# Performance work log

Measured on AMD Instinct MI355X. Metric: run time of the kernel, lower is better.

## Reference

```python
import jax, jax.numpy as jnp
import numpy as np

EPS = 0.1  # entropic regularization epsilon
N, F, R, H = 512, 32, 8, 128


def setup_inputs() -> dict:
    key = jax.random.key(0)
    ks = jax.random.split(key, 9)
    s0 = 1.0 / np.sqrt(F + R)
    sh = 1.0 / np.sqrt(H)
    return {
        "X": jax.random.normal(ks[0], (N, F), jnp.float32),
        "U": jax.random.normal(ks[1], (N, R), jnp.float32),
        "Y": jax.random.normal(ks[2], (N, R), jnp.float32),
        "Wx": jax.random.normal(ks[3], (F, H), jnp.float32) * s0,
        "Wy": jax.random.normal(ks[4], (R, H), jnp.float32) * s0,
        "b0": jnp.zeros((H,), jnp.float32),
        "W1": jax.random.normal(ks[5], (H, H), jnp.float32) * sh,
        "b1": jnp.zeros((H,), jnp.float32),
        "W2": jax.random.normal(ks[6], (H, H), jnp.float32) * sh,
        "b2": jnp.zeros((H,), jnp.float32),
        "Wout": jax.random.normal(ks[7], (H, 1), jnp.float32) * sh,
        "bout": jnp.zeros((1,), jnp.float32),
    }


def _mlp_tail(h, W1, b1, W2, b2, Wout, bout):
    h = jax.nn.softplus(h @ W1 + b1)
    h = jax.nn.softplus(h @ W2 + b2)
    return h @ Wout + bout  # [..., 1]


def reference(X, U, Y, Wx, Wy, b0, W1, b1, W2, b2, Wout, bout):
    n = X.shape[0]
    # ---- estimate_psi (potential net estimates 'y' side directly) ----
    h_row = jax.nn.softplus(X @ Wx + Y @ Wy + b0)              # [n, H]
    psi = _mlp_tail(h_row, W1, b1, W2, b2, Wout, bout)         # [n, 1]
    # ---- estimate_phi: entropic dual over all (X_i, Y_j) pairs ----
    # First-layer pre-activation built by broadcast-sum instead of concat.
    h_pair = jax.nn.softplus((X @ Wx)[:, None, :] + (Y @ Wy)[None, :, :] + b0)  # [n, n, H]
    psi_vals = _mlp_tail(h_pair, W1, b1, W2, b2, Wout, bout)[..., 0]            # [n, n]
    cost = U @ Y.T                                             # [n, n]
    slack = cost - psi_vals
    m = jnp.max(slack, axis=1, keepdims=True)                  # [n, 1]
    lme = jax.nn.logsumexp((slack - m) / EPS, axis=1, keepdims=True) \
          - jnp.log(jnp.asarray(n, slack.dtype)) + m / EPS
    phi = EPS * lme                                            # [n, 1]
    return jnp.mean(phi) + jnp.mean(psi)
```

## Files before the change

### kernel.cpp

```cpp
#include <hip/hip_runtime.h>
#include <hip/hip_bf16.h>
#include <math.h>

#define NN 512
#define HH 128
#define FF 32
#define RR 8
#define EPSV 0.1f
#define INV_EPS 10.0f
#define LOG2E 1.4426950408889634f
#define LN2 0.6931471805599453f
#define K2E (INV_EPS * LOG2E)

typedef unsigned short ushort_t;
typedef __attribute__((ext_vector_type(8))) short bf16x8;
typedef __attribute__((ext_vector_type(4))) float f32x4;
typedef __attribute__((ext_vector_type(4))) unsigned int u32x4;
typedef __attribute__((ext_vector_type(2))) unsigned int u32x2;

__device__ __forceinline__ float g2(float t) {
    return fmaxf(t, 0.f) + __log2f(1.f + __builtin_amdgcn_exp2f(-fabsf(t)));
}
__device__ __forceinline__ ushort_t f2b(float f) {
    unsigned u = __float_as_uint(f);
    return (ushort_t)((u + 0x7fffu + ((u >> 16) & 1u)) >> 16);
}
__device__ __forceinline__ float b2f(ushort_t h) {
    return __uint_as_float(((unsigned)h) << 16);
}
__device__ __forceinline__ unsigned pk2(float a, float b) {
    __hip_bfloat162 h = __float22bfloat162_rn(make_float2(a, b));
    return *reinterpret_cast<unsigned*>(&h);
}

__global__ __launch_bounds__(256) void prep_kernel(
    const float* __restrict__ X, const float* __restrict__ Y,
    const float* __restrict__ Wx, const float* __restrict__ Wy,
    const float* __restrict__ b0, const float* __restrict__ W1, const float* __restrict__ W2,
    const float* __restrict__ b1, const float* __restrict__ b2, const float* __restrict__ Wout,
    ushort_t* __restrict__ Wt1b, ushort_t* __restrict__ Wt2b,
    ushort_t* __restrict__ XWxb, ushort_t* __restrict__ YWyb,
    float* __restrict__ b1e, float* __restrict__ b2e, float* __restrict__ WoutE) {
    int gid = blockIdx.x * 256 + threadIdx.x;
    if (gid < 32768) {
        int sel = gid >> 14;
        int idx = gid & 16383;
        int n = idx >> 7, k = idx & 127;
        (sel ? Wt2b : Wt1b)[idx] = f2b((sel ? W2 : W1)[k * HH + n]);
    } else if (gid < 98304) {
        int g = gid - 32768;
        int i = g >> 7, h = g & 127;
        float s = b0[h];
#pragma unroll
        for (int f = 0; f < FF; ++f) s += X[i * FF + f] * Wx[f * HH + h];
        XWxb[g] = f2b(s * LOG2E);
    } else if (gid < 163840) {
        int g = gid - 98304;
        int i = g >> 7, h = g & 127;
        float s = 0.f;
#pragma unroll
        for (int r = 0; r < RR; ++r) s += Y[i * RR + r] * Wy[r * HH + h];
        YWyb[g] = f2b(s * LOG2E);
    } else if (gid < 163968) {
        b1e[gid - 163840] = b1[gid - 163840] * LOG2E;
    } else if (gid < 164096) {
        b2e[gid - 163968] = b2[gid - 163968] * LOG2E;
    } else if (gid < 164224) {
        WoutE[gid - 164096] = Wout[gid - 164096] * LN2;
    }
}

__device__ __forceinline__ void layer_flip(
    const ushort_t* __restrict__ Hin, const ushort_t* __restrict__ WtG,
    const float* __restrict__ bias, f32x4 acc[2][4], int r16, int g4, int wv) {
    const int hbase = wv * 32 + g4 * 4;
#pragma unroll
    for (int mt = 0; mt < 2; ++mt) {
        float4 bb = *(const float4*)&bias[hbase + mt * 16];
#pragma unroll
        for (int nt = 0; nt < 4; ++nt) {
            acc[mt][nt][0] = bb.x; acc[mt][nt][1] = bb.y;
            acc[mt][nt][2] = bb.z; acc[mt][nt][3] = bb.w;
        }
    }
    bf16x8 afr[2][4];
#pragma unroll
    for (int mt = 0; mt < 2; ++mt)
#pragma unroll
        for (int ks = 0; ks < 4; ++ks)
            afr[mt][ks] = *(const bf16x8*)&WtG[(wv * 32 + mt * 16 + r16) * HH + ks * 32 + g4 * 8];
#pragma unroll
    for (int ks = 0; ks < 4; ++ks) {
        const int kb = ks * 32 + g4 * 8;
#pragma unroll
        for (int nt = 0; nt < 4; ++nt) {
            const int j = nt * 16 + r16;
            bf16x8 bfr = *(const bf16x8*)&Hin[j * HH + (kb ^ ((j & 7) << 3))];
            acc[0][nt] = __builtin_amdgcn_mfma_f32_16x16x32_bf16(afr[0][ks], bfr, acc[0][nt], 0, 0, 0);
            acc[1][nt] = __builtin_amdgcn_mfma_f32_16x16x32_bf16(afr[1][ks], bfr, acc[1][nt], 0, 0, 0);
        }
    }
}

__global__ __launch_bounds__(256, 2) void pair_kernel(
    const ushort_t* __restrict__ XWxb, const ushort_t* __restrict__ YWyb,
    const ushort_t* __restrict__ Wt1b, const ushort_t* __restrict__ Wt2b,
    const float* __restrict__ U, const float* __restrict__ Y,
    const float* __restrict__ b1e, const float* __restrict__ b2e,
    const float* __restrict__ WoutE, const float* __restrict__ bout,
    float* __restrict__ psi_arr, float* __restrict__ Mp, float* __restrict__ Sp) {
    __shared__ ushort_t Hs0[64 * HH];
    __shared__ ushort_t Hs1[64 * HH];
    __shared__ float psum[4][64];

    const int i = blockIdx.x;
    const int half = blockIdx.y;
    const int t = threadIdx.x;
    const int wv = t >> 6;
    const int r16 = t & 15;
    const int g4 = (t >> 4) & 3;
    const int srow = t >> 4;
    const float boutv = bout[0];

    float axf[8];
    {
        bf16x8 axv = *(const bf16x8*)&XWxb[i * HH + r16 * 8];
#pragma unroll
        for (int e = 0; e < 8; ++e) axf[e] = b2f((ushort_t)axv[e]);
    }
    float costr[4];
    {
        const float4 u0 = *(const float4*)&U[i * RR];
        const float4 u1 = *(const float4*)&U[i * RR + 4];
#pragma unroll
        for (int c = 0; c < 4; ++c) {
            const int j = half * 256 + c * 64 + (t & 63);
            const float4 y0 = *(const float4*)&Y[j * RR];
            const float4 y1 = *(const float4*)&Y[j * RR + 4];
            costr[c] = u0.x * y0.x + u0.y * y0.y + u0.z * y0.z + u0.w * y0.w +
                       u1.x * y1.x + u1.y * y1.y + u1.z * y1.z + u1.w * y1.w;
        }
    }
    bf16x8 afr1[2][4];
#pragma unroll
    for (int mt = 0; mt < 2; ++mt)
#pragma unroll
        for (int ks = 0; ks < 4; ++ks)
            afr1[mt][ks] = *(const bf16x8*)&Wt1b[(wv * 32 + mt * 16 + r16) * HH + ks * 32 + g4 * 8];
    float4 bias1h[2];
    bias1h[0] = *(const float4*)&b1e[wv * 32 + g4 * 4];
    bias1h[1] = *(const float4*)&b1e[wv * 32 + 16 + g4 * 4];
    float4 woutr[2];
    woutr[0] = *(const float4*)&WoutE[wv * 32 + g4 * 4];
    woutr[1] = *(const float4*)&WoutE[wv * 32 + 16 + g4 * 4];

    float m_l = -INFINITY, s_l = 0.f;
    f32x4 acc[2][4];
    bf16x8 pf[4];

#pragma unroll
    for (int s = 0; s < 4; ++s)
        pf[s] = *(const bf16x8*)&YWyb[(half * 256 + s * 16 + srow) * HH + r16 * 8];

#pragma unroll
    for (int c = 0; c < 4; ++c) {
        const int j0 = half * 256 + c * 64;
#pragma unroll
        for (int s = 0; s < 4; ++s) {
            const int p = s * 16 + srow;
            const bf16x8 yv = pf[s];
            unsigned pk[4];
#pragma unroll
            for (int e = 0; e < 4; ++e) {
                float v0 = g2(axf[2 * e]     + b2f((ushort_t)yv[2 * e]));
                float v1 = g2(axf[2 * e + 1] + b2f((ushort_t)yv[2 * e + 1]));
                pk[e] = pk2(v0, v1);
            }
            *(u32x4*)&Hs0[p * HH + ((r16 ^ (p & 7)) << 3)] = *(u32x4*)pk;
        }
        __syncthreads();
        if (c < 3) {
#pragma unroll
            for (int s = 0; s < 4; ++s)
                pf[s] = *(const bf16x8*)&YWyb[(j0 + 64 + s * 16 + srow) * HH + r16 * 8];
        }
#pragma unroll
        for (int mt = 0; mt < 2; ++mt)
#pragma unroll
            for (int nt = 0; nt < 4; ++nt) {
                acc[mt][nt][0] = bias1h[mt].x; acc[mt][nt][1] = bias1h[mt].y;
                acc[mt][nt][2] = bias1h[mt].z; acc[mt][nt][3] = bias1h[mt].w;
            }
#pragma unroll
        for (int ks = 0; ks < 4; ++ks) {
            const int kb = ks * 32 + g4 * 8;
#pragma unroll
            for (int nt = 0; nt < 4; ++nt) {
                const int j = nt * 16 + r16;
                bf16x8 bfr = *(const bf16x8*)&Hs0[j * HH + (kb ^ ((j & 7) << 3))];
                acc[0][nt] = __builtin_amdgcn_mfma_f32_16x16x32_bf16(afr1[0][ks], bfr, acc[0][nt], 0, 0, 0);
                acc[1][nt] = __builtin_amdgcn_mfma_f32_16x16x32_bf16(afr1[1][ks], bfr, acc[1][nt], 0, 0, 0);
            }
        }
#pragma unroll
        for (int mt = 0; mt < 2; ++mt) {
            const int hb = wv * 32 + mt * 16 + g4 * 4;
#pragma unroll
            for (int nt = 0; nt < 4; ++nt) {
                const int j = nt * 16 + r16;
                u32x2 wv2;
                wv2[0] = pk2(g2(acc[mt][nt][0]), g2(acc[mt][nt][1]));
                wv2[1] = pk2(g2(acc[mt][nt][2]), g2(acc[mt][nt][3]));
                *(u32x2*)&Hs1[j * HH + (hb ^ ((j & 7) << 3))] = wv2;
            }
        }
        __syncthreads();
        layer_flip(Hs1, Wt2b, b2e, acc, r16, g4, wv);
        {
            float part[4] = {0.f, 0.f, 0.f, 0.f};
#pragma unroll
            for (int mt = 0; mt < 2; ++mt) {
                const float wr[4] = {woutr[mt].x, woutr[mt].y, woutr[mt].z, woutr[mt].w};
#pragma unroll
                for (int r = 0; r < 4; ++r) {
                    const float wgt = wr[r];
#pragma unroll
                    for (int nt = 0; nt < 4; ++nt)
                        part[nt] += g2(acc[mt][nt][r]) * wgt;
                }
            }
#pragma unroll
            for (int nt = 0; nt < 4; ++nt) {
                part[nt] += __shfl_xor(part[nt], 16);
                part[nt] += __shfl_xor(part[nt], 32);
            }
            if (g4 == 0) {
#pragma unroll
                for (int nt = 0; nt < 4; ++nt) psum[wv][nt * 16 + r16] = part[nt];
            }
        }
        __syncthreads();
        if (t < 64) {
            const float psi = boutv + psum[0][t] + psum[1][t] + psum[2][t] + psum[3][t];
            const int j = j0 + t;
            const float sv = costr[c] - psi;
            const float mn = fmaxf(m_l, sv);
            s_l = s_l * __builtin_amdgcn_exp2f((m_l - mn) * K2E) +
                  __builtin_amdgcn_exp2f((sv - mn) * K2E);
            m_l = mn;
            if (j == i) psi_arr[i] = psi;
        }
    }
    if (t < 64) {
        float M = m_l;
#pragma unroll
        for (int o = 1; o < 64; o <<= 1) M = fmaxf(M, __shfl_xor(M, o));
        float S = s_l * __builtin_amdgcn_exp2f((m_l - M) * K2E);
#pragma unroll
        for (int o = 1; o < 64; o <<= 1) S += __shfl_xor(S, o);
        if (t == 0) {
            Mp[i * 2 + half] = M;
            Sp[i * 2 + half] = S;
        }
    }
}

__global__ __launch_bounds__(512) void finalize_kernel(
    const float* __restrict__ psi_arr, const float* __restrict__ Mp,
    const float* __restrict__ Sp, float* __restrict__ out) {
    __shared__ float red[8];
    const int t = threadIdx.x;
    const float M0 = Mp[2 * t], M1 = Mp[2 * t + 1];
    const float S0 = Sp[2 * t], S1 = Sp[2 * t + 1];
    const float Mg = fmaxf(M0, M1);
    const float S = S0 * __expf((M0 - Mg) * INV_EPS) + S1 * __expf((M1 - Mg) * INV_EPS);
    const float phi = EPSV * (__logf(S) - __logf((float)NN)) + Mg;
    float v = phi + psi_arr[t];
#pragma unroll
    for (int o = 1; o < 64; o <<= 1) v += __shfl_xor(v, o);
    if ((t & 63) == 0) red[t >> 6] = v;
    __syncthreads();
    if (t == 0) {
        float tot = 0.f;
#pragma unroll
        for (int w = 0; w < 8; ++w) tot += red[w];
        out[0] = tot / (float)NN;
    }
}

extern "C" void kernel_launch(void* const* d_in, const int* in_sizes, int n_in,
                              void* d_out, int out_size, void* d_ws, size_t ws_size,
                              hipStream_t stream) {
    (void)in_sizes; (void)n_in; (void)out_size; (void)ws_size;
    const float* X    = (const float*)d_in[0];
    const float* U    = (const float*)d_in[1];
    const float* Y    = (const float*)d_in[2];
    const float* Wx   = (const float*)d_in[3];
    const float* Wy   = (const float*)d_in[4];
    const float* b0   = (const float*)d_in[5];
    const float* W1   = (const float*)d_in[6];
    const float* b1   = (const float*)d_in[7];
    const float* W2   = (const float*)d_in[8];
    const float* b2   = (const float*)d_in[9];
    const float* Wout = (const float*)d_in[10];
    const float* bout = (const float*)d_in[11];
    float* out = (float*)d_out;

    char* ws = (char*)d_ws;
    ushort_t* Wt1b    = (ushort_t*)(ws);
    ushort_t* Wt2b    = (ushort_t*)(ws + 32768);
    ushort_t* XWxb    = (ushort_t*)(ws + 65536);
    ushort_t* YWyb    = (ushort_t*)(ws + 196608);
    float*    psi_arr = (float*)(ws + 327680);
    float*    Mp      = (float*)(ws + 329728);
    float*    Sp      = (float*)(ws + 333824);
    float*    b1e     = (float*)(ws + 337920);
    float*    b2e     = (float*)(ws + 338432);
    float*    WoutE   = (float*)(ws + 338944);

    prep_kernel<<<642, 256, 0, stream>>>(X, Y, Wx, Wy, b0, W1, W2, b1, b2, Wout,
                                         Wt1b, Wt2b, XWxb, YWyb, b1e, b2e, WoutE);
    pair_kernel<<<dim3(NN, 2), 256, 0, stream>>>(XWxb, YWyb, Wt1b, Wt2b, U, Y,
                                                 b1e, b2e, WoutE, bout, psi_arr, Mp, Sp);
    finalize_kernel<<<1, 512, 0, stream>>>(psi_arr, Mp, Sp, out);
}
```

Measured before the change: 56.69 us.

## Split pair kernel into 64-column blocks and approximate softplus log with polynomial

```diff
diff --git a/kernel.cpp b/kernel.cpp
--- a/kernel.cpp
+++ b/kernel.cpp
@@ -12,6 +12,11 @@
 #define LN2 0.6931471805599453f
 #define K2E (INV_EPS * LOG2E)
 
+#define PC1 1.437284f
+#define PC2 (-0.672862f)
+#define PC3 0.315362f
+#define PC4 (-0.0799600f)
+
 typedef unsigned short ushort_t;
 typedef __attribute__((ext_vector_type(8))) short bf16x8;
 typedef __attribute__((ext_vector_type(4))) float f32x4;
@@ -19,7 +24,9 @@
 typedef __attribute__((ext_vector_type(2))) unsigned int u32x2;
 
 __device__ __forceinline__ float g2(float t) {
-    return fmaxf(t, 0.f) + __log2f(1.f + __builtin_amdgcn_exp2f(-fabsf(t)));
+    const float u = __builtin_amdgcn_exp2f(-fabsf(t));
+    const float p = u * (PC1 + u * (PC2 + u * (PC3 + u * PC4)));
+    return fmaxf(t, 0.f) + p;
 }
 __device__ __forceinline__ ushort_t f2b(float f) {
     unsigned u = __float_as_uint(f);
@@ -114,7 +121,8 @@
     __shared__ float psum[4][64];
 
     const int i = blockIdx.x;
-    const int half = blockIdx.y;
+    const int q = blockIdx.y;
+    const int j0 = q * 64;
     const int t = threadIdx.x;
     const int wv = t >> 6;
     const int r16 = t & 15;
@@ -128,18 +136,15 @@
 #pragma unroll
         for (int e = 0; e < 8; ++e) axf[e] = b2f((ushort_t)axv[e]);
     }
-    float costr[4];
+    float cost;
     {
+        const int j = j0 + (t & 63);
         const float4 u0 = *(const float4*)&U[i * RR];
         const float4 u1 = *(const float4*)&U[i * RR + 4];
-#pragma unroll
-        for (int c = 0; c < 4; ++c) {
-            const int j = half * 256 + c * 64 + (t & 63);
-            const float4 y0 = *(const float4*)&Y[j * RR];
-            const float4 y1 = *(const float4*)&Y[j * RR + 4];
-            costr[c] = u0.x * y0.x + u0.y * y0.y + u0.z * y0.z + u0.w * y0.w +
-                       u1.x * y1.x + u1.y * y1.y + u1.z * y1.z + u1.w * y1.w;
-        }
+        const float4 y0 = *(const float4*)&Y[j * RR];
+        const float4 y1 = *(const float4*)&Y[j * RR + 4];
+        cost = u0.x * y0.x + u0.y * y0.y + u0.z * y0.z + u0.w * y0.w +
+               u1.x * y1.x + u1.y * y1.y + u1.z * y1.z + u1.w * y1.w;
     }
     bf16x8 afr1[2][4];
 #pragma unroll
@@ -154,113 +159,94 @@
     woutr[0] = *(const float4*)&WoutE[wv * 32 + g4 * 4];
     woutr[1] = *(const float4*)&WoutE[wv * 32 + 16 + g4 * 4];
 
-    float m_l = -INFINITY, s_l = 0.f;
+#pragma unroll
+    for (int s = 0; s < 4; ++s) {
+        const int p = s * 16 + srow;
+        bf16x8 yv = *(const bf16x8*)&YWyb[(j0 + p) * HH + r16 * 8];
+        unsigned pk[4];
+#pragma unroll
+        for (int e = 0; e < 4; ++e) {
+            float v0 = g2(axf[2 * e]     + b2f((ushort_t)yv[2 * e]));
+            float v1 = g2(axf[2 * e + 1] + b2f((ushort_t)yv[2 * e + 1]));
+            pk[e] = pk2(v0, v1);
+        }
+        *(u32x4*)&Hs0[p * HH + ((r16 ^ (p & 7)) << 3)] = *(u32x4*)pk;
+    }
+    __syncthreads();
+
     f32x4 acc[2][4];
-    bf16x8 pf[4];
-
-#pragma unroll
-    for (int s = 0; s < 4; ++s)
-        pf[s] = *(const bf16x8*)&YWyb[(half * 256 + s * 16 + srow) * HH + r16 * 8];
-
-#pragma unroll
-    for (int c = 0; c < 4; ++c) {
-        const int j0 = half * 256 + c * 64;
-#pragma unroll
-        for (int s = 0; s < 4; ++s) {
-            const int p = s * 16 + srow;
-            const bf16x8 yv = pf[s];
-            unsigned pk[4];
-#pragma unroll
-            for (int e = 0; e < 4; ++e) {
-                float v0 = g2(axf[2 * e]     + b2f((ushort_t)yv[2 * e]));
-                float v1 = g2(axf[2 * e + 1] + b2f((ushort_t)yv[2 * e + 1]));
-                pk[e] = pk2(v0, v1);
+#pragma unroll
+    for (int mt = 0; mt < 2; ++mt)
+#pragma unroll
+        for (int nt = 0; nt < 4; ++nt) {
+            acc[mt][nt][0] = bias1h[mt].x; acc[mt][nt][1] = bias1h[mt].y;
+            acc[mt][nt][2] = bias1h[mt].z; acc[mt][nt][3] = bias1h[mt].w;
+        }
+#pragma unroll
+    for (int ks = 0; ks < 4; ++ks) {
+        const int kb = ks * 32 + g4 * 8;
+#pragma unroll
+        for (int nt = 0; nt < 4; ++nt) {
+            const int j = nt * 16 + r16;
+            bf16x8 bfr = *(const bf16x8*)&Hs0[j * HH + (kb ^ ((j & 7) << 3))];
+            acc[0][nt] = __builtin_amdgcn_mfma_f32_16x16x32_bf16(afr1[0][ks], bfr, acc[0][nt], 0, 0, 0);
+            acc[1][nt] = __builtin_amdgcn_mfma_f32_16x16x32_bf16(afr1[1][ks], bfr, acc[1][nt], 0, 0, 0);
+        }
+    }
+#pragma unroll
+    for (int mt = 0; mt < 2; ++mt) {
+        const int hb = wv * 32 + mt * 16 + g4 * 4;
+#pragma unroll
+        for (int nt = 0; nt < 4; ++nt) {
+            const int j = nt * 16 + r16;
+            u32x2 wv2;
+            wv2[0] = pk2(g2(acc[mt][nt][0]), g2(acc[mt][nt][1]));
+            wv2[1] = pk2(g2(acc[mt][nt][2]), g2(acc[mt][nt][3]));
+            *(u32x2*)&Hs1[j * HH + (hb ^ ((j & 7) << 3))] = wv2;
+        }
+    }
+    __syncthreads();
+
+    layer_flip(Hs1, Wt2b, b2e, acc, r16, g4, wv);
+    {
+        float part[4] = {0.f, 0.f, 0.f, 0.f};
+#pragma unroll
+        for (int mt = 0; mt < 2; ++mt) {
+            const float wr[4] = {woutr[mt].x, woutr[mt].y, woutr[mt].z, woutr[mt].w};
+#pragma unroll
+            for (int r = 0; r < 4; ++r) {
+                const float wgt = wr[r];
+#pragma unroll
+                for (int nt = 0; nt < 4; ++nt)
+                    part[nt] += g2(acc[mt][nt][r]) * wgt;
             }
-            *(u32x4*)&Hs0[p * HH + ((r16 ^ (p & 7)) << 3)] = *(u32x4*)pk;
-        }
-        __syncthreads();
-        if (c < 3) {
-#pragma unroll
-            for (int s = 0; s < 4; ++s)
-                pf[s] = *(const bf16x8*)&YWyb[(j0 + 64 + s * 16 + srow) * HH + r16 * 8];
-        }
-#pragma unroll
-        for (int mt = 0; mt < 2; ++mt)
-#pragma unroll
-            for (int nt = 0; nt < 4; ++nt) {
-                acc[mt][nt][0] = bias1h[mt].x; acc[mt][nt][1] = bias1h[mt].y;
-                acc[mt][nt][2] = bias1h[mt].z; acc[mt][nt][3] = bias1h[mt].w;
-            }
-#pragma unroll
-        for (int ks = 0; ks < 4; ++ks) {
-            const int kb = ks * 32 + g4 * 8;
-#pragma unroll
-            for (int nt = 0; nt < 4; ++nt) {
-                const int j = nt * 16 + r16;
-                bf16x8 bfr = *(const bf16x8*)&Hs0[j * HH + (kb ^ ((j & 7) << 3))];
-                acc[0][nt] = __builtin_amdgcn_mfma_f32_16x16x32_bf16(afr1[0][ks], bfr, acc[0][nt], 0, 0, 0);
-                acc[1][nt] = __builtin_amdgcn_mfma_f32_16x16x32_bf16(afr1[1][ks], bfr, acc[1][nt], 0, 0, 0);
-            }
-        }
-#pragma unroll
-        for (int mt = 0; mt < 2; ++mt) {
-            const int hb = wv * 32 + mt * 16 + g4 * 4;
-#pragma unroll
-            for (int nt = 0; nt < 4; ++nt) {
-                const int j = nt * 16 + r16;
-                u32x2 wv2;
-                wv2[0] = pk2(g2(acc[mt][nt][0]), g2(acc[mt][nt][1]));
-                wv2[1] = pk2(g2(acc[mt][nt][2]), g2(acc[mt][nt][3]));
-                *(u32x2*)&Hs1[j * HH + (hb ^ ((j & 7) << 3))] = wv2;
-            }
-        }
-        __syncthreads();
-        layer_flip(Hs1, Wt2b, b2e, acc, r16, g4, wv);
-        {
-            float part[4] = {0.f, 0.f, 0.f, 0.f};
-#pragma unroll
-            for (int mt = 0; mt < 2; ++mt) {
-                const float wr[4] = {woutr[mt].x, woutr[mt].y, woutr[mt].z, woutr[mt].w};
-#pragma unroll
-                for (int r = 0; r < 4; ++r) {
-                    const float wgt = wr[r];
-#pragma unroll
-                    for (int nt = 0; nt < 4; ++nt)
-                        part[nt] += g2(acc[mt][nt][r]) * wgt;
-                }
-            }
-#pragma unroll
-            for (int nt = 0; nt < 4; ++nt) {
-                part[nt] += __shfl_xor(part[nt], 16);
-                part[nt] += __shfl_xor(part[nt], 32);
-            }
-            if (g4 == 0) {
-#pragma unroll
-                for (int nt = 0; nt < 4; ++nt) psum[wv][nt * 16 + r16] = part[nt];
-            }
-        }
-        __syncthreads();
-        if (t < 64) {
-            const float psi = boutv + psum[0][t] + psum[1][t] + psum[2][t] + psum[3][t];
-            const int j = j0 + t;
-            const float sv = costr[c] - psi;
-            const float mn = fmaxf(m_l, sv);
-            s_l = s_l * __builtin_amdgcn_exp2f((m_l - mn) * K2E) +
-                  __builtin_amdgcn_exp2f((sv - mn) * K2E);
-            m_l = mn;
-            if (j == i) psi_arr[i] = psi;
-        }
-    }
+        }
+#pragma unroll
+        for (int nt = 0; nt < 4; ++nt) {
+            part[nt] += __shfl_xor(part[nt], 16);
+            part[nt] += __shfl_xor(part[nt], 32);
+        }
+        if (g4 == 0) {
+#pragma unroll
+            for (int nt = 0; nt < 4; ++nt) psum[wv][nt * 16 + r16] = part[nt];
+        }
+    }
+    __syncthreads();
+
     if (t < 64) {
-        float M = m_l;
+        const float psi = boutv + psum[0][t] + psum[1][t] + psum[2][t] + psum[3][t];
+        const int j = j0 + t;
+        if (j == i) psi_arr[i] = psi;
+        const float sv = cost - psi;
+        float M = sv;
 #pragma unroll
         for (int o = 1; o < 64; o <<= 1) M = fmaxf(M, __shfl_xor(M, o));
-        float S = s_l * __builtin_amdgcn_exp2f((m_l - M) * K2E);
+        float S = __builtin_amdgcn_exp2f((sv - M) * K2E);
 #pragma unroll
         for (int o = 1; o < 64; o <<= 1) S += __shfl_xor(S, o);
         if (t == 0) {
-            Mp[i * 2 + half] = M;
-            Sp[i * 2 + half] = S;
+            Mp[i * 8 + q] = M;
+            Sp[i * 8 + q] = S;
         }
     }
 }
@@ -270,10 +256,15 @@
     const float* __restrict__ Sp, float* __restrict__ out) {
     __shared__ float red[8];
     const int t = threadIdx.x;
-    const float M0 = Mp[2 * t], M1 = Mp[2 * t + 1];
-    const float S0 = Sp[2 * t], S1 = Sp[2 * t + 1];
-    const float Mg = fmaxf(M0, M1);
-    const float S = S0 * __expf((M0 - Mg) * INV_EPS) + S1 * __expf((M1 - Mg) * INV_EPS);
+    float Mq[8], Sq[8];
+#pragma unroll
+    for (int q = 0; q < 8; ++q) { Mq[q] = Mp[t * 8 + q]; Sq[q] = Sp[t * 8 + q]; }
+    float Mg = Mq[0];
+#pragma unroll
+    for (int q = 1; q < 8; ++q) Mg = fmaxf(Mg, Mq[q]);
+    float S = 0.f;
+#pragma unroll
+    for (int q = 0; q < 8; ++q) S += Sq[q] * __builtin_amdgcn_exp2f((Mq[q] - Mg) * K2E);
     const float phi = EPSV * (__logf(S) - __logf((float)NN)) + Mg;
     float v = phi + psi_arr[t];
 #pragma unroll
@@ -313,14 +304,14 @@
     ushort_t* YWyb    = (ushort_t*)(ws + 196608);
     float*    psi_arr = (float*)(ws + 327680);
     float*    Mp      = (float*)(ws + 329728);
-    float*    Sp      = (float*)(ws + 333824);
-    float*    b1e     = (float*)(ws + 337920);
-    float*    b2e     = (float*)(ws + 338432);
-    float*    WoutE   = (float*)(ws + 338944);
+    float*    Sp      = (float*)(ws + 346112);
+    float*    b1e     = (float*)(ws + 362496);
+    float*    b2e     = (float*)(ws + 363008);
+    float*    WoutE   = (float*)(ws + 363520);
 
     prep_kernel<<<642, 256, 0, stream>>>(X, Y, Wx, Wy, b0, W1, W2, b1, b2, Wout,
                                          Wt1b, Wt2b, XWxb, YWyb, b1e, b2e, WoutE);
-    pair_kernel<<<dim3(NN, 2), 256, 0, stream>>>(XWxb, YWyb, Wt1b, Wt2b, U, Y,
+    pair_kernel<<<dim3(NN, 8), 256, 0, stream>>>(XWxb, YWyb, Wt1b, Wt2b, U, Y,
                                                  b1e, b2e, WoutE, bout, psi_arr, Mp, Sp);
     finalize_kernel<<<1, 512, 0, stream>>>(psi_arr, Mp, Sp, out);
 }
```

Measured after the change: 53.44 us. 1.06x faster.
